# Kernel tuning notes

Hardware: AMD Instinct MI355X
Metric: run time of the kernel (lower is better)

The kernel has to match this reference:

```python
import jax, jax.numpy as jnp
import numpy as np
from jax import lax

B, T, H, L = 128, 512, 1024, 32


def setup_inputs() -> dict:
    key = jax.random.key(0)
    ks = jax.random.split(key, 8)
    outputs = jax.random.normal(ks[0], (B, T, H), jnp.float32)
    labels = jax.random.randint(ks[1], (B, T), 0, L)
    mask = jnp.ones((B, T), dtype=bool)
    fc_w = jax.random.normal(ks[2], (L, H), jnp.float32) * 0.02  # nn.Linear weight [out,in]
    fc_b = jnp.zeros((L,), jnp.float32)
    # torchcrf initializes transitions ~ U(-0.1, 0.1)
    start_transitions = jax.random.uniform(ks[3], (L,), jnp.float32, -0.1, 0.1)
    end_transitions = jax.random.uniform(ks[4], (L,), jnp.float32, -0.1, 0.1)
    transitions = jax.random.uniform(ks[5], (L, L), jnp.float32, -0.1, 0.1)
    return dict(outputs=outputs, labels=labels, mask=mask, fc_w=fc_w, fc_b=fc_b,
                start_transitions=start_transitions, end_transitions=end_transitions,
                transitions=transitions)


def reference(outputs, labels, mask, fc_w, fc_b, start_transitions, end_transitions, transitions):
    # emissions: [B, T, L]
    emissions = jnp.einsum('bth,lh->btl', outputs, fc_w) + fc_b
    b_, t_, l_ = emissions.shape
    mf = mask.astype(emissions.dtype)

    # ---- numerator: score of gold path (vectorized over time) ----
    first_tags = labels[:, 0]
    em_scores = jnp.take_along_axis(emissions, labels[..., None], axis=2)[..., 0]  # [B,T]
    trans_scores = transitions[labels[:, :-1], labels[:, 1:]]                       # [B,T-1]
    numerator = (start_transitions[first_tags] + em_scores[:, 0]
                 + jnp.sum((trans_scores + em_scores[:, 1:]) * mf[:, 1:], axis=1))
    seq_ends = mask.sum(axis=1).astype(jnp.int32) - 1
    last_tags = jnp.take_along_axis(labels, seq_ends[:, None], axis=1)[:, 0]
    numerator = numerator + end_transitions[last_tags]

    # ---- denominator: forward algorithm (logsumexp recurrence) ----
    score0 = start_transitions + emissions[:, 0]          # [B,L]
    em_rest = jnp.swapaxes(emissions[:, 1:], 0, 1)        # [T-1,B,L]
    m_rest = jnp.swapaxes(mask[:, 1:], 0, 1)              # [T-1,B]

    def fwd_step(score, xs):
        em_t, m_t = xs
        nxt = jax.nn.logsumexp(score[:, :, None] + transitions[None] + em_t[:, None, :], axis=1)
        return jnp.where(m_t[:, None], nxt, score), None

    score, _ = lax.scan(fwd_step, score0, (em_rest, m_rest))
    denominator = jax.nn.logsumexp(score + end_transitions, axis=1)

    llh = numerator - denominator
    loss = -jnp.mean(llh)  # reduction='mean', negated in the module

    # ---- Viterbi decode ----
    idx_l = jnp.arange(l_)

    def vit_step(score, xs):
        em_t, m_t = xs
        bcast = score[:, :, None] + transitions[None]     # [B,L_prev,L_next]
        nxt = bcast.max(axis=1) + em_t
        idx = jnp.argmax(bcast, axis=1)
        idx = jnp.where(m_t[:, None], idx, idx_l[None, :])  # identity pointer on padded steps
        return jnp.where(m_t[:, None], nxt, score), idx

    vscore, history = lax.scan(vit_step, score0, (em_rest, m_rest))  # history: [T-1,B,L]
    last_tag = jnp.argmax(vscore + end_transitions, axis=1)          # [B]

    def back_step(tag, idx):
        prev = jnp.take_along_axis(idx, tag[:, None], axis=1)[:, 0]
        return prev, prev

    _, prevs = lax.scan(back_step, last_tag, history, reverse=True)  # [T-1,B]
    pred = jnp.concatenate([prevs, last_tag[None]], axis=0).T        # [B,T]
    return loss, pred
```

## Files before the change

kernel.cpp:

```cpp
#include <hip/hip_runtime.h>

#define Bn 128
#define Tn 512
#define Hn 1024
#define Ln 32
#define L2E 1.44269504088896340736f
#define LN2 0.69314718055994530942f

typedef unsigned short ushort_t;
typedef __attribute__((ext_vector_type(8))) short bf16x8;
typedef __attribute__((ext_vector_type(4))) float f32x4;

#if __has_builtin(__builtin_amdgcn_exp2f)
#define EXP2F(x) __builtin_amdgcn_exp2f(x)
#else
#define EXP2F(x) exp2f(x)
#endif
#if __has_builtin(__builtin_amdgcn_logf)
#define LOG2F(x) __builtin_amdgcn_logf(x)
#else
#define LOG2F(x) log2f(x)
#endif

__device__ __forceinline__ float rfirstf(float v) {
  return __int_as_float(__builtin_amdgcn_readfirstlane(__float_as_int(v)));
}
__device__ __forceinline__ float bpermf(int byteidx, float v) {
  return __int_as_float(__builtin_amdgcn_ds_bpermute(byteidx, __float_as_int(v)));
}

#define DPPX(x, CTRL)                                                          \
  __int_as_float(__builtin_amdgcn_update_dpp(                                  \
      0, __float_as_int(x), (CTRL), 0xF, 0xF, false))

__device__ __forceinline__ float cross32f(float x, int l) {
#if __has_builtin(__builtin_amdgcn_permlane32_swap)
  int xi = __float_as_int(x);
  auto pp = __builtin_amdgcn_permlane32_swap(xi, xi, false, false);
  return __int_as_float(pp[0] ^ pp[1] ^ xi);
#else
  return __int_as_float(
      __builtin_amdgcn_ds_bpermute(((l ^ 32) << 2), __float_as_int(x)));
#endif
}
__device__ __forceinline__ int swap16i(int x) {
#if __has_builtin(__builtin_amdgcn_permlane16_swap)
  auto pp = __builtin_amdgcn_permlane16_swap(x, x, false, false);
  return pp[0] ^ pp[1] ^ x;
#else
  return __builtin_amdgcn_ds_swizzle(x, 0x401F);
#endif
}
__device__ __forceinline__ float swap16f(float x) {
  return __int_as_float(swap16i(__float_as_int(x)));
}

#define GATHER16(BASE, G)                                                      \
  float G##0 = (BASE);                                                         \
  float G##1 = DPPX(G##0, 0xB1);                                               \
  float G##2 = DPPX(G##0, 0x4E), G##3 = DPPX(G##1, 0x4E);                      \
  float G##4 = DPPX(G##3, 0x141), G##5 = DPPX(G##2, 0x141),                    \
        G##6 = DPPX(G##1, 0x141), G##7 = DPPX(G##0, 0x141);                    \
  float G##8 = DPPX(G##7, 0x140), G##9 = DPPX(G##6, 0x140),                    \
        G##10 = DPPX(G##5, 0x140), G##11 = DPPX(G##4, 0x140),                  \
        G##12 = DPPX(G##3, 0x140), G##13 = DPPX(G##2, 0x140),                  \
        G##14 = DPPX(G##1, 0x140), G##15 = DPPX(G##0, 0x140);

__device__ __forceinline__ ushort_t f2bf(float f) {
  unsigned int x = __float_as_uint(f);
  unsigned int r = x + 0x7FFFu + ((x >> 16) & 1u);
  return (ushort_t)(r >> 16);
}

__global__ __launch_bounds__(256) void k_emissions(
    const float* __restrict__ outs, const float* __restrict__ fcw,
    const float* __restrict__ fcb, float* __restrict__ emis,
    float* __restrict__ loss0)
{
  if (blockIdx.x == 0 && threadIdx.x == 0) loss0[0] = 0.0f;
  __shared__ ushort_t wl[32 * 1032];
  __shared__ ushort_t xl[2][256 * 40];
  const int tid = threadIdx.x;
  const int rowBase = blockIdx.x << 8;

  {
    const int j = tid >> 3;
    const int kc = (tid & 7) << 7;
#pragma unroll
    for (int i = 0; i < 32; ++i) {
      float4 v = *(const float4*)&fcw[(size_t)j * Hn + kc + i * 4];
      ushort4 u;
      u.x = f2bf(v.x); u.y = f2bf(v.y); u.z = f2bf(v.z); u.w = f2bf(v.w);
      *(ushort4*)&wl[j * 1032 + kc + i * 4] = u;
    }
  }

#define STAGE_X(BUF, S)                                                        \
  {                                                                            \
    const float* src = outs + (size_t)(rowBase + tid) * Hn + (S) * 32;         \
    _Pragma("unroll")                                                          \
    for (int q = 0; q < 8; ++q) {                                              \
      float4 v = *(const float4*)(src + q * 4);                                \
      ushort4 u;                                                               \
      u.x = f2bf(v.x); u.y = f2bf(v.y); u.z = f2bf(v.z); u.w = f2bf(v.w);      \
      *(ushort4*)&xl[BUF][tid * 40 + q * 4] = u;                               \
    }                                                                          \
  }

  STAGE_X(0, 0)
  __syncthreads();

  const int l = tid & 63;
  const int wv = tid >> 6;
  const int wrow = wv << 6;
  const int lm = l & 15;
  const int koct = l >> 4;

  f32x4 acc[4][2];
#pragma unroll
  for (int mt = 0; mt < 4; ++mt)
#pragma unroll
    for (int nt = 0; nt < 2; ++nt) acc[mt][nt] = (f32x4){0.f, 0.f, 0.f, 0.f};

  for (int s = 0; s < 32; ++s) {
    const int buf = s & 1;
    if (s < 31) STAGE_X(buf ^ 1, s + 1)
    bf16x8 bf0 = *(const bf16x8*)&wl[(0 * 16 + lm) * 1032 + s * 32 + koct * 8];
    bf16x8 bf1 = *(const bf16x8*)&wl[(1 * 16 + lm) * 1032 + s * 32 + koct * 8];
#pragma unroll
    for (int mt = 0; mt < 4; ++mt) {
      bf16x8 af = *(const bf16x8*)&xl[buf][(wrow + mt * 16 + lm) * 40 + koct * 8];
      acc[mt][0] = __builtin_amdgcn_mfma_f32_16x16x32_bf16(af, bf0, acc[mt][0], 0, 0, 0);
      acc[mt][1] = __builtin_amdgcn_mfma_f32_16x16x32_bf16(af, bf1, acc[mt][1], 0, 0, 0);
    }
    __syncthreads();
  }
#undef STAGE_X

  float b0 = fcb[lm];
  float b1 = fcb[16 + lm];
#pragma unroll
  for (int mt = 0; mt < 4; ++mt)
#pragma unroll
    for (int r = 0; r < 4; ++r) {
      size_t row = (size_t)(rowBase + wrow + mt * 16 + koct * 4 + r);
      emis[row * 32 + lm] = acc[mt][0][r] + b0;
      emis[row * 32 + 16 + lm] = acc[mt][1][r] + b1;
    }
}

__global__ __launch_bounds__(64) void k_scan(
    const float* __restrict__ emis, const int* __restrict__ labels,
    const float* __restrict__ trans, const float* __restrict__ startT,
    const float* __restrict__ endT, float* __restrict__ d_out)
{
  __shared__ int histI[512 * 32];
  __shared__ int hist2[256 * 32];
  __shared__ int hist4[128 * 32];
  __shared__ int tagsL[512];
  const int l = threadIdx.x;
  const int colc = (l & 15) | ((l & 32) >> 1);
  const int cb = colc ^ (l & 16);

  if (blockIdx.x < Bn) {
    const int b = blockIdx.x;
    const float* eb = emis + (size_t)b * Tn * Ln;

    float num = 0.f;
#pragma unroll
    for (int q = 0; q < 8; ++q) {
      int tt = l + q * 64;
      int lab = labels[b * Tn + tt];
      num += eb[tt * Ln + lab];
      if (tt > 0) num += trans[labels[b * Tn + tt - 1] * Ln + lab];
      if (tt == 0) num += startT[lab];
      if (tt == Tn - 1) num += endT[lab];
    }
#pragma unroll
    for (int m = 1; m < 64; m <<= 1) num += __shfl_xor(num, m, 64);

    float w[16];
#pragma unroll
    for (int m = 0; m < 16; ++m)
      w[m] = EXP2F(trans[(cb ^ m) * Ln + colc] * L2E);

    float p = 0.f, C2 = 0.f;
    for (int ww = 0; ww < 16; ++ww) {
      float emr[32];
#pragma unroll
      for (int tp = 0; tp < 32; ++tp)
        emr[tp] = eb[(ww * 32 + tp) * 32 + colc];
      if (ww == 0) {
        float v0 = (startT[colc] + emr[0]) * L2E;
        float a0i = rfirstf(v0);
        C2 = a0i;
        p = EXP2F(v0 - a0i);
      }
#pragma unroll
      for (int tp = 0; tp < 32; ++tp) {
        if (ww == 0 && tp == 0) continue;
        float crx = cross32f(p, l);
        float base = (l & 16) ? crx : p;
        GATHER16(base, gf)
        float A0 = fmaf(gf3, w[3], fmaf(gf2, w[2], fmaf(gf1, w[1], gf0 * w[0])));
        float A1 = fmaf(gf7, w[7], fmaf(gf6, w[6], fmaf(gf5, w[5], gf4 * w[4])));
        float A2 = fmaf(gf11, w[11], fmaf(gf10, w[10], fmaf(gf9, w[9], gf8 * w[8])));
        float A3 = fmaf(gf15, w[15], fmaf(gf14, w[14], fmaf(gf13, w[13], gf12 * w[12])));
        float Sh = (A0 + A1) + (A2 + A3);
        float S = Sh + swap16f(Sh);
        p = S * EXP2F(emr[tp] * L2E);
        if ((tp & 3) == 3) {
          int pb = __float_as_int(rfirstf(p));
          int ke = (pb >> 23) & 0xff;
          C2 += (float)(ke - 127);
          p *= __int_as_float((unsigned)(254 - ke) << 23);
        }
      }
    }
    float ex = p * EXP2F(endT[colc] * L2E);
#pragma unroll
    for (int m = 1; m < 64; m <<= 1) ex += __shfl_xor(ex, m, 64);
    float den = (C2 + LOG2F(ex) - 1.0f) * LN2;
    float llh = num - den;
    if (l == 0) atomicAdd(d_out, -llh * (1.0f / (float)Bn));
  } else {
    const int b = blockIdx.x - Bn;
    const float* eb = emis + (size_t)b * Tn * Ln;

    float t16[16];
#pragma unroll
    for (int m = 0; m < 16; ++m) t16[m] = trans[(cb ^ m) * Ln + colc];

    float r = 0.f;
    for (int ww = 0; ww < 16; ++ww) {
      float emr[32];
#pragma unroll
      for (int tp = 0; tp < 32; ++tp)
        emr[tp] = eb[(ww * 32 + tp) * 32 + colc];
      if (ww == 0) r = startT[colc] + emr[0];
#pragma unroll
      for (int tp = 0; tp < 32; ++tp) {
        if (ww == 0 && tp == 0) continue;
        float crx = cross32f(r, l);
        float base = (l & 16) ? crx : r;
        GATHER16(base, gv)
        float e0 = gv0 + t16[0], e1 = gv1 + t16[1], e2 = gv2 + t16[2],
              e3 = gv3 + t16[3], e4 = gv4 + t16[4], e5 = gv5 + t16[5],
              e6 = gv6 + t16[6], e7 = gv7 + t16[7], e8 = gv8 + t16[8],
              e9 = gv9 + t16[9], e10 = gv10 + t16[10], e11 = gv11 + t16[11],
              e12 = gv12 + t16[12], e13 = gv13 + t16[13], e14 = gv14 + t16[14],
              e15 = gv15 + t16[15];
        float m0 = fmaxf(fmaxf(e0, e1), e2);
        float m1 = fmaxf(fmaxf(e3, e4), e5);
        float m2 = fmaxf(fmaxf(e6, e7), e8);
        float m3 = fmaxf(fmaxf(e9, e10), e11);
        float m4 = fmaxf(fmaxf(e12, e13), e14);
        float Mh = fmaxf(fmaxf(fmaxf(m0, m1), m2),
                         fmaxf(fmaxf(m3, m4), e15));
        int amh = 15;
        amh = (e14 == Mh) ? 14 : amh;
        amh = (e13 == Mh) ? 13 : amh;
        amh = (e12 == Mh) ? 12 : amh;
        amh = (e11 == Mh) ? 11 : amh;
        amh = (e10 == Mh) ? 10 : amh;
        amh = (e9 == Mh) ? 9 : amh;
        amh = (e8 == Mh) ? 8 : amh;
        amh = (e7 == Mh) ? 7 : amh;
        amh = (e6 == Mh) ? 6 : amh;
        amh = (e5 == Mh) ? 5 : amh;
        amh = (e4 == Mh) ? 4 : amh;
        amh = (e3 == Mh) ? 3 : amh;
        amh = (e2 == Mh) ? 2 : amh;
        amh = (e1 == Mh) ? 1 : amh;
        amh = (e0 == Mh) ? 0 : amh;
        int srch = cb ^ amh;
        float Mo = swap16f(Mh);
        int srco = swap16i(srch);
        bool tk = (Mo > Mh) || (Mo == Mh && srco < srch);
        float M = tk ? Mo : Mh;
        int st = tk ? srco : srch;
        const int tm1 = ww * 32 + tp - 1;
        histI[tm1 * 32 + (colc ^ (tm1 & 31))] = st;
        r = M + emr[tp];
      }
    }

    float mv = r + endT[colc];
    int mi = colc;
#define RED_STEP(PAT)                                                          \
    {                                                                          \
      float ov2 = __int_as_float(__builtin_amdgcn_ds_swizzle(__float_as_int(mv), PAT)); \
      int oi2 = __builtin_amdgcn_ds_swizzle(mi, PAT);                          \
      bool take = (ov2 > mv) || (ov2 == mv && oi2 < mi);                       \
      mv = take ? ov2 : mv;                                                    \
      mi = take ? oi2 : mi;                                                    \
    }
    RED_STEP(0x401F) RED_STEP(0x201F) RED_STEP(0x101F) RED_STEP(0x081F) RED_STEP(0x041F)
#undef RED_STEP
    {
      float ovx = bpermf((l ^ 32) << 2, mv);
      int oix = __builtin_amdgcn_ds_bpermute((l ^ 32) << 2, mi);
      bool take = (ovx > mv) || (ovx == mv && oix < mi);
      mv = take ? ovx : mv;
      mi = take ? oix : mi;
    }
    const int lastTag = mi;
    __syncthreads();

#pragma unroll 4
    for (int e = l; e < 255 * 32; e += 64) {
      int t2 = e >> 5, jx = e & 31, t = t2 << 1;
      int a = histI[(t + 1) * 32 + (jx ^ ((t + 1) & 31))];
      int bb = histI[t * 32 + (a ^ (t & 31))];
      hist2[t2 * 32 + (jx ^ (t2 & 31))] = bb;
    }
    __syncthreads();
#pragma unroll 4
    for (int e = l; e < 127 * 32; e += 64) {
      int t4 = e >> 5, jx = e & 31;
      int a = hist2[(2 * t4 + 1) * 32 + (jx ^ ((2 * t4 + 1) & 31))];
      int bb = hist2[(2 * t4) * 32 + (a ^ ((2 * t4) & 31))];
      hist4[t4 * 32 + (jx ^ (t4 & 31))] = bb;
    }
    __syncthreads();

    int tag = lastTag;
    if (l == 0) tagsL[511] = tag;
    tag = histI[510 * 32 + (tag ^ (510 & 31))];
    if (l == 0) tagsL[510] = tag;
    int cur = hist2[254 * 32 + (tag ^ (254 & 31))];
    if (l == 0) tagsL[508] = cur;
    for (int t4 = 126; t4 >= 0; --t4) {
      cur = hist4[t4 * 32 + (cur ^ (t4 & 31))];
      if (l == 0) tagsL[t4 << 2] = cur;
    }
    __syncthreads();
    for (int e = l; e < 127; e += 64) {
      int t2 = 2 * e + 1, t = t2 << 1;
      int tp2 = tagsL[t + 2];
      tagsL[t] = hist2[t2 * 32 + (tp2 ^ (t2 & 31))];
    }
    __syncthreads();
    for (int e = l; e < 255; e += 64) {
      int t = 2 * e + 1;
      int tp1 = tagsL[t + 1];
      tagsL[t] = histI[t * 32 + (tp1 ^ (t & 31))];
    }
    __syncthreads();

    float* predf = d_out + 1 + (size_t)b * Tn;
#pragma unroll
    for (int q = 0; q < 8; ++q) {
      int t = q * 64 + l;
      predf[t] = (float)tagsL[t];
    }
  }
}

extern "C" void kernel_launch(void* const* d_in, const int* in_sizes, int n_in,
                              void* d_out, int out_size, void* d_ws, size_t ws_size,
                              hipStream_t stream) {
  const float* outs = (const float*)d_in[0];
  const int* labels = (const int*)d_in[1];
  const float* fcw = (const float*)d_in[3];
  const float* fcb = (const float*)d_in[4];
  const float* stT = (const float*)d_in[5];
  const float* enT = (const float*)d_in[6];
  const float* trn = (const float*)d_in[7];
  float* emis = (float*)d_ws;
  float* out = (float*)d_out;

  hipLaunchKernelGGL(k_emissions, dim3(256), dim3(256), 0, stream,
                     outs, fcw, fcb, emis, out);
  hipLaunchKernelGGL(k_scan, dim3(256), dim3(64), 0, stream,
                     emis, labels, trn, stT, enT, out);
}
```

Baseline: 224.9 us.

## Interleave forward and Viterbi recurrences in one wave; double GEMM block threads

The scan kernel previously ran the forward (logsumexp) recurrence and the Viterbi recurrence in separate blocks, 256 blocks in total. It now runs both dependent chains interleaved in the same 64-thread block, one block per batch. The independent chains can hide each other's DPP and transcendental latency and the emission loads are shared. The cost is a longer per-block critical path with only 128 blocks on the GPU. Separately, the emissions GEMM kernel now uses 512 threads per block with smaller per-wave tiles, giving more waves per CU for latency hiding.

```diff
diff --git a/kernel.cpp b/kernel.cpp
--- a/kernel.cpp
+++ b/kernel.cpp
@@ -72,7 +72,7 @@
   return (ushort_t)(r >> 16);
 }
 
-__global__ __launch_bounds__(256) void k_emissions(
+__global__ __launch_bounds__(512) void k_emissions(
     const float* __restrict__ outs, const float* __restrict__ fcw,
     const float* __restrict__ fcb, float* __restrict__ emis,
     float* __restrict__ loss0)
@@ -84,10 +84,10 @@
   const int rowBase = blockIdx.x << 8;
 
   {
-    const int j = tid >> 3;
-    const int kc = (tid & 7) << 7;
-#pragma unroll
-    for (int i = 0; i < 32; ++i) {
+    const int j = tid >> 4;
+    const int kc = (tid & 15) << 6;
+#pragma unroll
+    for (int i = 0; i < 16; ++i) {
       float4 v = *(const float4*)&fcw[(size_t)j * Hn + kc + i * 4];
       ushort4 u;
       u.x = f2bf(v.x); u.y = f2bf(v.y); u.z = f2bf(v.z); u.w = f2bf(v.w);
@@ -97,13 +97,15 @@
 
 #define STAGE_X(BUF, S)                                                        \
   {                                                                            \
-    const float* src = outs + (size_t)(rowBase + tid) * Hn + (S) * 32;         \
+    const int row_ = tid >> 1;                                                 \
+    const int kh_ = (tid & 1) << 4;                                            \
+    const float* src = outs + (size_t)(rowBase + row_) * Hn + (S) * 32 + kh_;  \
     _Pragma("unroll")                                                          \
-    for (int q = 0; q < 8; ++q) {                                              \
+    for (int q = 0; q < 4; ++q) {                                              \
       float4 v = *(const float4*)(src + q * 4);                                \
       ushort4 u;                                                               \
       u.x = f2bf(v.x); u.y = f2bf(v.y); u.z = f2bf(v.z); u.w = f2bf(v.w);      \
-      *(ushort4*)&xl[BUF][tid * 40 + q * 4] = u;                               \
+      *(ushort4*)&xl[BUF][row_ * 40 + kh_ + q * 4] = u;                        \
     }                                                                          \
   }
 
@@ -112,13 +114,13 @@
 
   const int l = tid & 63;
   const int wv = tid >> 6;
-  const int wrow = wv << 6;
+  const int wrow = wv << 5;
   const int lm = l & 15;
   const int koct = l >> 4;
 
-  f32x4 acc[4][2];
-#pragma unroll
-  for (int mt = 0; mt < 4; ++mt)
+  f32x4 acc[2][2];
+#pragma unroll
+  for (int mt = 0; mt < 2; ++mt)
 #pragma unroll
     for (int nt = 0; nt < 2; ++nt) acc[mt][nt] = (f32x4){0.f, 0.f, 0.f, 0.f};
 
@@ -128,7 +130,7 @@
     bf16x8 bf0 = *(const bf16x8*)&wl[(0 * 16 + lm) * 1032 + s * 32 + koct * 8];
     bf16x8 bf1 = *(const bf16x8*)&wl[(1 * 16 + lm) * 1032 + s * 32 + koct * 8];
 #pragma unroll
-    for (int mt = 0; mt < 4; ++mt) {
+    for (int mt = 0; mt < 2; ++mt) {
       bf16x8 af = *(const bf16x8*)&xl[buf][(wrow + mt * 16 + lm) * 40 + koct * 8];
       acc[mt][0] = __builtin_amdgcn_mfma_f32_16x16x32_bf16(af, bf0, acc[mt][0], 0, 0, 0);
       acc[mt][1] = __builtin_amdgcn_mfma_f32_16x16x32_bf16(af, bf1, acc[mt][1], 0, 0, 0);
@@ -140,7 +142,7 @@
   float b0 = fcb[lm];
   float b1 = fcb[16 + lm];
 #pragma unroll
-  for (int mt = 0; mt < 4; ++mt)
+  for (int mt = 0; mt < 2; ++mt)
 #pragma unroll
     for (int r = 0; r < 4; ++r) {
       size_t row = (size_t)(rowBase + wrow + mt * 16 + koct * 4 + r);
@@ -161,86 +163,50 @@
   const int l = threadIdx.x;
   const int colc = (l & 15) | ((l & 32) >> 1);
   const int cb = colc ^ (l & 16);
-
-  if (blockIdx.x < Bn) {
-    const int b = blockIdx.x;
-    const float* eb = emis + (size_t)b * Tn * Ln;
-
-    float num = 0.f;
-#pragma unroll
-    for (int q = 0; q < 8; ++q) {
-      int tt = l + q * 64;
-      int lab = labels[b * Tn + tt];
-      num += eb[tt * Ln + lab];
-      if (tt > 0) num += trans[labels[b * Tn + tt - 1] * Ln + lab];
-      if (tt == 0) num += startT[lab];
-      if (tt == Tn - 1) num += endT[lab];
-    }
-#pragma unroll
-    for (int m = 1; m < 64; m <<= 1) num += __shfl_xor(num, m, 64);
-
-    float w[16];
-#pragma unroll
-    for (int m = 0; m < 16; ++m)
-      w[m] = EXP2F(trans[(cb ^ m) * Ln + colc] * L2E);
-
-    float p = 0.f, C2 = 0.f;
-    for (int ww = 0; ww < 16; ++ww) {
-      float emr[32];
-#pragma unroll
-      for (int tp = 0; tp < 32; ++tp)
-        emr[tp] = eb[(ww * 32 + tp) * 32 + colc];
-      if (ww == 0) {
-        float v0 = (startT[colc] + emr[0]) * L2E;
-        float a0i = rfirstf(v0);
-        C2 = a0i;
-        p = EXP2F(v0 - a0i);
-      }
-#pragma unroll
-      for (int tp = 0; tp < 32; ++tp) {
-        if (ww == 0 && tp == 0) continue;
-        float crx = cross32f(p, l);
-        float base = (l & 16) ? crx : p;
-        GATHER16(base, gf)
-        float A0 = fmaf(gf3, w[3], fmaf(gf2, w[2], fmaf(gf1, w[1], gf0 * w[0])));
-        float A1 = fmaf(gf7, w[7], fmaf(gf6, w[6], fmaf(gf5, w[5], gf4 * w[4])));
-        float A2 = fmaf(gf11, w[11], fmaf(gf10, w[10], fmaf(gf9, w[9], gf8 * w[8])));
-        float A3 = fmaf(gf15, w[15], fmaf(gf14, w[14], fmaf(gf13, w[13], gf12 * w[12])));
-        float Sh = (A0 + A1) + (A2 + A3);
-        float S = Sh + swap16f(Sh);
-        p = S * EXP2F(emr[tp] * L2E);
-        if ((tp & 3) == 3) {
-          int pb = __float_as_int(rfirstf(p));
-          int ke = (pb >> 23) & 0xff;
-          C2 += (float)(ke - 127);
-          p *= __int_as_float((unsigned)(254 - ke) << 23);
-        }
-      }
-    }
-    float ex = p * EXP2F(endT[colc] * L2E);
-#pragma unroll
-    for (int m = 1; m < 64; m <<= 1) ex += __shfl_xor(ex, m, 64);
-    float den = (C2 + LOG2F(ex) - 1.0f) * LN2;
-    float llh = num - den;
-    if (l == 0) atomicAdd(d_out, -llh * (1.0f / (float)Bn));
-  } else {
-    const int b = blockIdx.x - Bn;
-    const float* eb = emis + (size_t)b * Tn * Ln;
-
-    float t16[16];
-#pragma unroll
-    for (int m = 0; m < 16; ++m) t16[m] = trans[(cb ^ m) * Ln + colc];
-
-    float r = 0.f;
-    for (int ww = 0; ww < 16; ++ww) {
-      float emr[32];
-#pragma unroll
-      for (int tp = 0; tp < 32; ++tp)
-        emr[tp] = eb[(ww * 32 + tp) * 32 + colc];
-      if (ww == 0) r = startT[colc] + emr[0];
-#pragma unroll
-      for (int tp = 0; tp < 32; ++tp) {
-        if (ww == 0 && tp == 0) continue;
+  const int b = blockIdx.x;
+  const float* eb = emis + (size_t)b * Tn * Ln;
+
+  float num = 0.f;
+#pragma unroll
+  for (int q = 0; q < 8; ++q) {
+    int tt = l + q * 64;
+    int lab = labels[b * Tn + tt];
+    num += eb[tt * Ln + lab];
+    if (tt > 0) num += trans[labels[b * Tn + tt - 1] * Ln + lab];
+    if (tt == 0) num += startT[lab];
+    if (tt == Tn - 1) num += endT[lab];
+  }
+#pragma unroll
+  for (int m = 1; m < 64; m <<= 1) num += __shfl_xor(num, m, 64);
+
+  float w[16], t16[16];
+#pragma unroll
+  for (int m = 0; m < 16; ++m) {
+    float tv = trans[(cb ^ m) * Ln + colc];
+    t16[m] = tv;
+    w[m] = EXP2F(tv * L2E);
+  }
+
+  float p = 0.f, C2 = 0.f;
+  float r = 0.f;
+
+  for (int ww = 0; ww < 32; ++ww) {
+    float emr[16];
+#pragma unroll
+    for (int tp = 0; tp < 16; ++tp)
+      emr[tp] = eb[(ww * 16 + tp) * 32 + colc];
+    if (ww == 0) {
+      float v0 = (startT[colc] + emr[0]) * L2E;
+      float a0i = rfirstf(v0);
+      C2 = a0i;
+      p = EXP2F(v0 - a0i);
+      r = startT[colc] + emr[0];
+    }
+#pragma unroll
+    for (int tp = 0; tp < 16; ++tp) {
+      if (ww == 0 && tp == 0) continue;
+      const int tt = ww * 16 + tp;
+      {
         float crx = cross32f(r, l);
         float base = (l & 16) ? crx : r;
         GATHER16(base, gv)
@@ -279,81 +245,108 @@
         bool tk = (Mo > Mh) || (Mo == Mh && srco < srch);
         float M = tk ? Mo : Mh;
         int st = tk ? srco : srch;
-        const int tm1 = ww * 32 + tp - 1;
+        const int tm1 = tt - 1;
         histI[tm1 * 32 + (colc ^ (tm1 & 31))] = st;
         r = M + emr[tp];
       }
-    }
-
-    float mv = r + endT[colc];
-    int mi = colc;
+      {
+        float crx = cross32f(p, l);
+        float base = (l & 16) ? crx : p;
+        GATHER16(base, gf)
+        float A0 = fmaf(gf3, w[3], fmaf(gf2, w[2], fmaf(gf1, w[1], gf0 * w[0])));
+        float A1 = fmaf(gf7, w[7], fmaf(gf6, w[6], fmaf(gf5, w[5], gf4 * w[4])));
+        float A2 = fmaf(gf11, w[11], fmaf(gf10, w[10], fmaf(gf9, w[9], gf8 * w[8])));
+        float A3 = fmaf(gf15, w[15], fmaf(gf14, w[14], fmaf(gf13, w[13], gf12 * w[12])));
+        float Sh = (A0 + A1) + (A2 + A3);
+        float S = Sh + swap16f(Sh);
+        p = S * EXP2F(emr[tp] * L2E);
+        if ((tt & 3) == 3) {
+          int pb = __float_as_int(rfirstf(p));
+          int ke = (pb >> 23) & 0xff;
+          C2 += (float)(ke - 127);
+          p *= __int_as_float((unsigned)(254 - ke) << 23);
+        }
+      }
+    }
+  }
+
+  {
+    float ex = p * EXP2F(endT[colc] * L2E);
+#pragma unroll
+    for (int m = 1; m < 64; m <<= 1) ex += __shfl_xor(ex, m, 64);
+    float den = (C2 + LOG2F(ex) - 1.0f) * LN2;
+    float llh = num - den;
+    if (l == 0) atomicAdd(d_out, -llh * (1.0f / (float)Bn));
+  }
+
+  float mv = r + endT[colc];
+  int mi = colc;
 #define RED_STEP(PAT)                                                          \
-    {                                                                          \
-      float ov2 = __int_as_float(__builtin_amdgcn_ds_swizzle(__float_as_int(mv), PAT)); \
-      int oi2 = __builtin_amdgcn_ds_swizzle(mi, PAT);                          \
-      bool take = (ov2 > mv) || (ov2 == mv && oi2 < mi);                       \
-      mv = take ? ov2 : mv;                                                    \
-      mi = take ? oi2 : mi;                                                    \
-    }
-    RED_STEP(0x401F) RED_STEP(0x201F) RED_STEP(0x101F) RED_STEP(0x081F) RED_STEP(0x041F)
+  {                                                                            \
+    float ov2 = __int_as_float(__builtin_amdgcn_ds_swizzle(__float_as_int(mv), PAT)); \
+    int oi2 = __builtin_amdgcn_ds_swizzle(mi, PAT);                            \
+    bool take = (ov2 > mv) || (ov2 == mv && oi2 < mi);                         \
+    mv = take ? ov2 : mv;                                                      \
+    mi = take ? oi2 : mi;                                                      \
+  }
+  RED_STEP(0x401F) RED_STEP(0x201F) RED_STEP(0x101F) RED_STEP(0x081F) RED_STEP(0x041F)
 #undef RED_STEP
-    {
-      float ovx = bpermf((l ^ 32) << 2, mv);
-      int oix = __builtin_amdgcn_ds_bpermute((l ^ 32) << 2, mi);
-      bool take = (ovx > mv) || (ovx == mv && oix < mi);
-      mv = take ? ovx : mv;
-      mi = take ? oix : mi;
-    }
-    const int lastTag = mi;
-    __syncthreads();
+  {
+    float ovx = bpermf((l ^ 32) << 2, mv);
+    int oix = __builtin_amdgcn_ds_bpermute((l ^ 32) << 2, mi);
+    bool take = (ovx > mv) || (ovx == mv && oix < mi);
+    mv = take ? ovx : mv;
+    mi = take ? oix : mi;
+  }
+  const int lastTag = mi;
+  __syncthreads();
 
 #pragma unroll 4
-    for (int e = l; e < 255 * 32; e += 64) {
-      int t2 = e >> 5, jx = e & 31, t = t2 << 1;
-      int a = histI[(t + 1) * 32 + (jx ^ ((t + 1) & 31))];
-      int bb = histI[t * 32 + (a ^ (t & 31))];
-      hist2[t2 * 32 + (jx ^ (t2 & 31))] = bb;
-    }
-    __syncthreads();
+  for (int e = l; e < 255 * 32; e += 64) {
+    int t2 = e >> 5, jx = e & 31, t = t2 << 1;
+    int a = histI[(t + 1) * 32 + (jx ^ ((t + 1) & 31))];
+    int bb = histI[t * 32 + (a ^ (t & 31))];
+    hist2[t2 * 32 + (jx ^ (t2 & 31))] = bb;
+  }
+  __syncthreads();
 #pragma unroll 4
-    for (int e = l; e < 127 * 32; e += 64) {
-      int t4 = e >> 5, jx = e & 31;
-      int a = hist2[(2 * t4 + 1) * 32 + (jx ^ ((2 * t4 + 1) & 31))];
-      int bb = hist2[(2 * t4) * 32 + (a ^ ((2 * t4) & 31))];
-      hist4[t4 * 32 + (jx ^ (t4 & 31))] = bb;
-    }
-    __syncthreads();
-
-    int tag = lastTag;
-    if (l == 0) tagsL[511] = tag;
-    tag = histI[510 * 32 + (tag ^ (510 & 31))];
-    if (l == 0) tagsL[510] = tag;
-    int cur = hist2[254 * 32 + (tag ^ (254 & 31))];
-    if (l == 0) tagsL[508] = cur;
-    for (int t4 = 126; t4 >= 0; --t4) {
-      cur = hist4[t4 * 32 + (cur ^ (t4 & 31))];
-      if (l == 0) tagsL[t4 << 2] = cur;
-    }
-    __syncthreads();
-    for (int e = l; e < 127; e += 64) {
-      int t2 = 2 * e + 1, t = t2 << 1;
-      int tp2 = tagsL[t + 2];
-      tagsL[t] = hist2[t2 * 32 + (tp2 ^ (t2 & 31))];
-    }
-    __syncthreads();
-    for (int e = l; e < 255; e += 64) {
-      int t = 2 * e + 1;
-      int tp1 = tagsL[t + 1];
-      tagsL[t] = histI[t * 32 + (tp1 ^ (t & 31))];
-    }
-    __syncthreads();
-
-    float* predf = d_out + 1 + (size_t)b * Tn;
-#pragma unroll
-    for (int q = 0; q < 8; ++q) {
-      int t = q * 64 + l;
-      predf[t] = (float)tagsL[t];
-    }
+  for (int e = l; e < 127 * 32; e += 64) {
+    int t4 = e >> 5, jx = e & 31;
+    int a = hist2[(2 * t4 + 1) * 32 + (jx ^ ((2 * t4 + 1) & 31))];
+    int bb = hist2[(2 * t4) * 32 + (a ^ ((2 * t4) & 31))];
+    hist4[t4 * 32 + (jx ^ (t4 & 31))] = bb;
+  }
+  __syncthreads();
+
+  int tag = lastTag;
+  if (l == 0) tagsL[511] = tag;
+  tag = histI[510 * 32 + (tag ^ (510 & 31))];
+  if (l == 0) tagsL[510] = tag;
+  int cur = hist2[254 * 32 + (tag ^ (254 & 31))];
+  if (l == 0) tagsL[508] = cur;
+  for (int t4 = 126; t4 >= 0; --t4) {
+    cur = hist4[t4 * 32 + (cur ^ (t4 & 31))];
+    if (l == 0) tagsL[t4 << 2] = cur;
+  }
+  __syncthreads();
+  for (int e = l; e < 127; e += 64) {
+    int t2 = 2 * e + 1, t = t2 << 1;
+    int tp2 = tagsL[t + 2];
+    tagsL[t] = hist2[t2 * 32 + (tp2 ^ (t2 & 31))];
+  }
+  __syncthreads();
+  for (int e = l; e < 255; e += 64) {
+    int t = 2 * e + 1;
+    int tp1 = tagsL[t + 1];
+    tagsL[t] = histI[t * 32 + (tp1 ^ (t & 31))];
+  }
+  __syncthreads();
+
+  float* predf = d_out + 1 + (size_t)b * Tn;
+#pragma unroll
+  for (int q = 0; q < 8; ++q) {
+    int t = q * 64 + l;
+    predf[t] = (float)tagsL[t];
   }
 }
 
@@ -370,8 +363,8 @@
   float* emis = (float*)d_ws;
   float* out = (float*)d_out;
 
-  hipLaunchKernelGGL(k_emissions, dim3(256), dim3(256), 0, stream,
+  hipLaunchKernelGGL(k_emissions, dim3(256), dim3(512), 0, stream,
                      outs, fcw, fcb, emis, out);
-  hipLaunchKernelGGL(k_scan, dim3(256), dim3(64), 0, stream,
+  hipLaunchKernelGGL(k_scan, dim3(128), dim3(64), 0, stream,
                      emis, labels, trn, stT, enT, out);
 }
```

Result: slower. 272.8 us (+21.3%).
